# Kernel tuning notes

Measured on AMD Instinct MI355X. Metric: run time of the kernel, lower is better.

Reference implementation:

```python
import jax, jax.numpy as jnp
import numpy as np

C_M = 256
C = 32
N_HEAD = 8
N_SEQ = 256
N_RES = 384


def setup_inputs() -> dict:
    key = jax.random.key(0)
    ks = jax.random.split(key, 10)
    s = 1.0 / np.sqrt(C_M)
    so = 1.0 / np.sqrt(N_HEAD * C)
    return {
        "m": jax.random.normal(ks[0], (N_SEQ, N_RES, C_M), dtype=jnp.float32),
        "ln_gamma": jnp.ones((C_M,), jnp.float32),
        "ln_beta": jnp.zeros((C_M,), jnp.float32),
        "Wq": jax.random.normal(ks[1], (C_M, N_HEAD * C), jnp.float32) * s,
        "Wk": jax.random.normal(ks[2], (C_M, N_HEAD * C), jnp.float32) * s,
        "Wv": jax.random.normal(ks[3], (C_M, N_HEAD * C), jnp.float32) * s,
        "Wg": jax.random.normal(ks[4], (C_M, N_HEAD * C), jnp.float32) * s,
        "bg": jnp.zeros((N_HEAD * C,), jnp.float32),
        "Wo": jax.random.normal(ks[5], (N_HEAD * C, C_M), jnp.float32) * so,
        "bo": jnp.zeros((C_M,), jnp.float32),
    }


def reference(m, ln_gamma, ln_beta, Wq, Wk, Wv, Wg, bg, Wo, bo):
    # LayerNorm over c_m
    mu = jnp.mean(m, axis=-1, keepdims=True)
    var = jnp.mean(jnp.square(m - mu), axis=-1, keepdims=True)
    x = (m - mu) * jax.lax.rsqrt(var + 1e-5) * ln_gamma + ln_beta

    # attention over N_seq axis (attn_dim=-3): move it next to features
    xt = jnp.swapaxes(x, 0, 1)  # (R, S, c_m)
    R, S = xt.shape[0], xt.shape[1]

    def heads(t):  # (R, S, H*c) -> (R, H, S, c)
        return jnp.swapaxes(t.reshape(R, S, N_HEAD, C), 1, 2)

    q = heads(xt @ Wq)
    k = heads(xt @ Wk)
    v = heads(xt @ Wv)

    logits = jnp.einsum("rhqc,rhkc->rhqk", q, k) / jnp.sqrt(jnp.asarray(C, x.dtype))
    attn = jax.nn.softmax(logits, axis=-1)
    o = jnp.einsum("rhqk,rhkc->rhqc", attn, v)  # (R, H, S, c)
    o = jnp.swapaxes(o, 1, 2).reshape(R, S, N_HEAD * C)

    g = jax.nn.sigmoid(xt @ Wg + bg)  # (R, S, H*c)
    out = (g * o) @ Wo + bo  # (R, S, c_m)
    return jnp.swapaxes(out, 0, 1)  # back to (S, R, c_m)
```

## Files before the change

### kernel.cpp

```cpp
#include <hip/hip_runtime.h>
#include <hip/hip_bf16.h>

#define NSEQ 256
#define NRES 384
#define CM   256
#define NH   8
#define HC   32

typedef __bf16 bf16x8_t __attribute__((ext_vector_type(8)));
typedef __bf16 bf16x4_t __attribute__((ext_vector_type(4)));
typedef float  f32x4_t  __attribute__((ext_vector_type(4)));

static __device__ __forceinline__ f32x4_t mfma16(bf16x8_t a, bf16x8_t b, f32x4_t c) {
    return __builtin_amdgcn_mfma_f32_16x16x32_bf16(a, b, c, 0, 0, 0);
}

static __device__ __forceinline__ bf16x4_t to_bf4(f32x4_t v) {
    bf16x4_t o;
    o[0] = (__bf16)v[0]; o[1] = (__bf16)v[1];
    o[2] = (__bf16)v[2]; o[3] = (__bf16)v[3];
    return o;
}

__global__ __launch_bounds__(256) void wprep_kernel(
        const float* __restrict__ wq, const float* __restrict__ wk,
        const float* __restrict__ wv, const float* __restrict__ wg,
        const float* __restrict__ wo, __bf16* __restrict__ wt) {
    const float* src;
    switch (blockIdx.y) {
        case 0: src = wq; break; case 1: src = wk; break;
        case 2: src = wv; break; case 3: src = wg; break;
        default: src = wo; break;
    }
    __bf16* dst = wt + (size_t)blockIdx.y * (CM * CM);
    int n  = blockIdx.x * 16 + (threadIdx.x >> 4);
    int k0 = (threadIdx.x & 15) * 16;
    #pragma unroll
    for (int kk = 0; kk < 16; ++kk) {
        int k = k0 + kk;
        dst[n * CM + k] = (__bf16)src[k * CM + n];
    }
}

__global__ __launch_bounds__(256) void ln_kernel(
        const float* __restrict__ m, const float* __restrict__ gamma,
        const float* __restrict__ beta, __bf16* __restrict__ x) {
    int w = threadIdx.x >> 6, lane = threadIdx.x & 63;
    int row = blockIdx.x * 4 + w;
    const float4 mv = *reinterpret_cast<const float4*>(m + (size_t)row * CM + lane * 4);
    float s1 = mv.x + mv.y + mv.z + mv.w;
    float s2 = mv.x * mv.x + mv.y * mv.y + mv.z * mv.z + mv.w * mv.w;
    #pragma unroll
    for (int d = 1; d < 64; d <<= 1) {
        s1 += __shfl_xor(s1, d);
        s2 += __shfl_xor(s2, d);
    }
    float mu  = s1 * (1.0f / CM);
    float var = s2 * (1.0f / CM) - mu * mu;
    float rs  = rsqrtf(var + 1e-5f);
    const float4 gv = *reinterpret_cast<const float4*>(gamma + lane * 4);
    const float4 bv = *reinterpret_cast<const float4*>(beta + lane * 4);
    int s = row / NRES;
    int r = row - s * NRES;
    int drow = r * NSEQ + s;
    bf16x4_t o;
    o[0] = (__bf16)((mv.x - mu) * rs * gv.x + bv.x);
    o[1] = (__bf16)((mv.y - mu) * rs * gv.y + bv.y);
    o[2] = (__bf16)((mv.z - mu) * rs * gv.z + bv.z);
    o[3] = (__bf16)((mv.w - mu) * rs * gv.w + bv.w);
    *reinterpret_cast<bf16x4_t*>(x + (size_t)drow * CM + lane * 4) = o;
}

__global__ __launch_bounds__(256, 2) void attn_kernel(
        const __bf16* __restrict__ x, const __bf16* __restrict__ wt,
        const float* __restrict__ bg, __bf16* __restrict__ go) {
    const int KRW = 40;
    const int VRW = 264;

    __shared__ __align__(16) char smem[57856];
    __bf16* k_s  = reinterpret_cast<__bf16*>(smem);
    __bf16* q_s  = reinterpret_cast<__bf16*>(smem + 20480);
    __bf16* v_sT = reinterpret_cast<__bf16*>(smem + 40960);

    int tid = threadIdx.x;
    int w = tid >> 6, lane = tid & 63;
    int l15 = lane & 15, g4 = lane >> 4;

    int bid = blockIdx.x;
    int nid = (bid & 7) * 384 + (bid >> 3);
    int r = nid >> 3, h = nid & 7;

    const __bf16* xr = x + (size_t)r * NSEQ * CM;

    const f32x4_t zf = {0.0f, 0.0f, 0.0f, 0.0f};
    f32x4_t acc[4][4][2];
    #pragma unroll
    for (int wi = 0; wi < 4; ++wi)
        #pragma unroll
        for (int mt = 0; mt < 4; ++mt)
            #pragma unroll
            for (int ct = 0; ct < 2; ++ct) acc[wi][mt][ct] = zf;

    #pragma unroll
    for (int kb = 0; kb < 8; ++kb) {
        bf16x8_t a[4];
        #pragma unroll
        for (int mt = 0; mt < 4; ++mt)
            a[mt] = *reinterpret_cast<const bf16x8_t*>(
                xr + (w * 64 + mt * 16 + l15) * CM + kb * 32 + g4 * 8);
        #pragma unroll
        for (int wi = 0; wi < 4; ++wi) {
            const __bf16* wslice = wt + (size_t)wi * (CM * CM) + (h * HC) * CM;
            bf16x8_t b[2];
            #pragma unroll
            for (int ct = 0; ct < 2; ++ct)
                b[ct] = *reinterpret_cast<const bf16x8_t*>(
                    wslice + (ct * 16 + l15) * CM + kb * 32 + g4 * 8);
            #pragma unroll
            for (int mt = 0; mt < 4; ++mt)
                #pragma unroll
                for (int ct = 0; ct < 2; ++ct)
                    acc[wi][mt][ct] = mfma16(a[mt], b[ct], acc[wi][mt][ct]);
        }
    }

    #pragma unroll
    for (int mt = 0; mt < 4; ++mt)
        #pragma unroll
        for (int ct = 0; ct < 2; ++ct) {
            #pragma unroll
            for (int i = 0; i < 4; ++i) {
                q_s[(w * 64 + mt * 16 + g4 * 4 + i) * KRW + ct * 16 + l15] =
                    (__bf16)acc[0][mt][ct][i];
                k_s[(w * 64 + mt * 16 + g4 * 4 + i) * KRW + ct * 16 + l15] =
                    (__bf16)acc[1][mt][ct][i];
            }
            *reinterpret_cast<bf16x4_t*>(
                v_sT + (ct * 16 + l15) * VRW + w * 64 + mt * 16 + g4 * 4) =
                to_bf4(acc[2][mt][ct]);
        }
    __syncthreads();

    bf16x8_t kf[16];
    #pragma unroll
    for (int kt = 0; kt < 16; ++kt)
        kf[kt] = *reinterpret_cast<const bf16x8_t*>(k_s + (kt * 16 + l15) * KRW + g4 * 8);
    bf16x8_t qf[4];
    #pragma unroll
    for (int qt = 0; qt < 4; ++qt)
        qf[qt] = *reinterpret_cast<const bf16x8_t*>(q_s + (w * 64 + qt * 16 + l15) * KRW + g4 * 8);
    __syncthreads();

    __bf16* p_s = reinterpret_cast<__bf16*>(smem + w * 8448);

    float bgv[2];
    bgv[0] = bg[h * HC + l15];
    bgv[1] = bg[h * HC + 16 + l15];
    const float scale = 0.17677669529663687f;

    #pragma unroll
    for (int qt = 0; qt < 4; ++qt) {
        f32x4_t sacc[16];
        #pragma unroll
        for (int kt = 0; kt < 16; ++kt) sacc[kt] = zf;
        #pragma unroll
        for (int kt = 0; kt < 16; ++kt) sacc[kt] = mfma16(kf[kt], qf[qt], sacc[kt]);

        float mx = -1e30f;
        #pragma unroll
        for (int kt = 0; kt < 16; ++kt)
            #pragma unroll
            for (int i = 0; i < 4; ++i) mx = fmaxf(mx, sacc[kt][i]);
        mx = fmaxf(mx, __shfl_xor(mx, 16));
        mx = fmaxf(mx, __shfl_xor(mx, 32));
        float sum = 0.0f;
        #pragma unroll
        for (int kt = 0; kt < 16; ++kt)
            #pragma unroll
            for (int i = 0; i < 4; ++i) {
                float e = __expf((sacc[kt][i] - mx) * scale);
                sacc[kt][i] = e;
                sum += e;
            }
        sum += __shfl_xor(sum, 16);
        sum += __shfl_xor(sum, 32);
        float inv = 1.0f / sum;

        #pragma unroll
        for (int kt = 0; kt < 16; ++kt) {
            bf16x4_t pv;
            #pragma unroll
            for (int i = 0; i < 4; ++i) pv[i] = (__bf16)(sacc[kt][i] * inv);
            *reinterpret_cast<bf16x4_t*>(p_s + l15 * VRW + kt * 16 + g4 * 4) = pv;
        }

        f32x4_t oacc[2];
        oacc[0] = zf; oacc[1] = zf;
        #pragma unroll
        for (int kb = 0; kb < 8; ++kb) {
            bf16x8_t pa = *reinterpret_cast<const bf16x8_t*>(p_s + l15 * VRW + kb * 32 + g4 * 8);
            #pragma unroll
            for (int ct = 0; ct < 2; ++ct) {
                bf16x8_t vb = *reinterpret_cast<const bf16x8_t*>(
                    v_sT + (ct * 16 + l15) * VRW + kb * 32 + g4 * 8);
                oacc[ct] = mfma16(pa, vb, oacc[ct]);
            }
        }

        #pragma unroll
        for (int ct = 0; ct < 2; ++ct)
            #pragma unroll
            for (int i = 0; i < 4; ++i) {
                float t  = acc[3][qt][ct][i] + bgv[ct];
                float gs = 1.0f / (1.0f + __expf(-t));
                int row  = r * NSEQ + w * 64 + qt * 16 + g4 * 4 + i;
                go[(size_t)row * CM + h * HC + ct * 16 + l15] = (__bf16)(gs * oacc[ct][i]);
            }
    }
}

__global__ __launch_bounds__(256, 2) void outgemm_kernel(
        const __bf16* __restrict__ go, const __bf16* __restrict__ wto,
        const float* __restrict__ bo, float* __restrict__ out) {
    int tid = threadIdx.x, w = tid >> 6, lane = tid & 63;
    int l15 = lane & 15, g4 = lane >> 4;
    int j0 = blockIdx.x * 64 + w * 16;
    const f32x4_t zf = {0.0f, 0.0f, 0.0f, 0.0f};
    f32x4_t acc[16];
    #pragma unroll
    for (int nt = 0; nt < 16; ++nt) acc[nt] = zf;
    #pragma unroll
    for (int kb = 0; kb < 8; ++kb) {
        bf16x8_t a = *reinterpret_cast<const bf16x8_t*>(
            go + (size_t)(j0 + l15) * CM + kb * 32 + g4 * 8);
        #pragma unroll
        for (int nt = 0; nt < 16; ++nt) {
            bf16x8_t b = *reinterpret_cast<const bf16x8_t*>(
                wto + (nt * 16 + l15) * CM + kb * 32 + g4 * 8);
            acc[nt] = mfma16(a, b, acc[nt]);
        }
    }
    #pragma unroll
    for (int nt = 0; nt < 16; ++nt) {
        float bias = bo[nt * 16 + l15];
        #pragma unroll
        for (int i = 0; i < 4; ++i) {
            int j = j0 + g4 * 4 + i;
            int s = j & (NSEQ - 1);
            int rr = j >> 8;
            out[((size_t)(s * NRES + rr)) * CM + nt * 16 + l15] = acc[nt][i] + bias;
        }
    }
}

extern "C" void kernel_launch(void* const* d_in, const int* in_sizes, int n_in,
                              void* d_out, int out_size, void* d_ws, size_t ws_size,
                              hipStream_t stream) {
    const float* m     = (const float*)d_in[0];
    const float* gamma = (const float*)d_in[1];
    const float* beta  = (const float*)d_in[2];
    const float* wq    = (const float*)d_in[3];
    const float* wk    = (const float*)d_in[4];
    const float* wv    = (const float*)d_in[5];
    const float* wg    = (const float*)d_in[6];
    const float* bg    = (const float*)d_in[7];
    const float* wo    = (const float*)d_in[8];
    const float* bo    = (const float*)d_in[9];

    char* ws = (char*)d_ws;
    const size_t X_OFF  = 1u << 20;
    const size_t GO_OFF = X_OFF + (size_t)NRES * NSEQ * CM * 2;
    const size_t NEED   = GO_OFF + (size_t)NRES * NSEQ * CM * 2;
    if (ws_size < NEED) return;

    __bf16* wt = (__bf16*)ws;
    __bf16* x  = (__bf16*)(ws + X_OFF);
    __bf16* go = (__bf16*)(ws + GO_OFF);

    wprep_kernel<<<dim3(16, 5), 256, 0, stream>>>(wq, wk, wv, wg, wo, wt);
    ln_kernel<<<(NSEQ * NRES) / 4, 256, 0, stream>>>(m, gamma, beta, x);
    attn_kernel<<<NRES * NH, 256, 0, stream>>>(x, wt, bg, go);
    outgemm_kernel<<<(NRES * NSEQ) / 64, 256, 0, stream>>>(go, wt + 4 * (CM * CM), bo, (float*)d_out);
}
```

Measured before the change: 309.0 us.

## Tile weight transpose, head-major gated output layout, exp2 softmax, MFMA priority

The weight-prep kernel now transposes through a shared-memory tile, so global reads and writes are coalesced instead of strided. The attention kernel writes the gated output in a head-major (r, h, s, c) layout so each head's stores are contiguous, and the output GEMM reads A fragments from that layout. Softmax and sigmoid use exp2 with the scale folded into an FMA. s_setprio is raised around the MFMA loops. These are several unrelated micro-optimizations bundled together; the weight prep is small, so most of any benefit would come from the store-layout change.

```diff
diff --git a/kernel.cpp b/kernel.cpp
--- a/kernel.cpp
+++ b/kernel.cpp
@@ -26,19 +26,27 @@
         const float* __restrict__ wq, const float* __restrict__ wk,
         const float* __restrict__ wv, const float* __restrict__ wg,
         const float* __restrict__ wo, __bf16* __restrict__ wt) {
+    __shared__ float tile[64][65];
     const float* src;
-    switch (blockIdx.y) {
+    switch (blockIdx.z) {
         case 0: src = wq; break; case 1: src = wk; break;
         case 2: src = wv; break; case 3: src = wg; break;
         default: src = wo; break;
     }
-    __bf16* dst = wt + (size_t)blockIdx.y * (CM * CM);
-    int n  = blockIdx.x * 16 + (threadIdx.x >> 4);
-    int k0 = (threadIdx.x & 15) * 16;
-    #pragma unroll
-    for (int kk = 0; kk < 16; ++kk) {
-        int k = k0 + kk;
-        dst[n * CM + k] = (__bf16)src[k * CM + n];
+    __bf16* dst = wt + (size_t)blockIdx.z * (CM * CM);
+    int k0 = blockIdx.x * 64;
+    int n0 = blockIdx.y * 64;
+    int lane = threadIdx.x & 63, wv2 = threadIdx.x >> 6;
+    #pragma unroll
+    for (int i = 0; i < 16; ++i) {
+        int kk = wv2 * 16 + i;
+        tile[kk][lane] = src[(size_t)(k0 + kk) * CM + n0 + lane];
+    }
+    __syncthreads();
+    #pragma unroll
+    for (int i = 0; i < 16; ++i) {
+        int nn = wv2 * 16 + i;
+        dst[(size_t)(n0 + nn) * CM + k0 + lane] = (__bf16)tile[lane][nn];
     }
 }
 
@@ -156,15 +164,20 @@
     float bgv[2];
     bgv[0] = bg[h * HC + l15];
     bgv[1] = bg[h * HC + 16 + l15];
-    const float scale = 0.17677669529663687f;
+    const float cs = 0.17677669529663687f * 1.4426950408889634f;
+    const float l2e = 1.4426950408889634f;
+
+    __bf16* gor = go + (((size_t)r * NH + h) * NSEQ) * HC;
 
     #pragma unroll
     for (int qt = 0; qt < 4; ++qt) {
         f32x4_t sacc[16];
         #pragma unroll
         for (int kt = 0; kt < 16; ++kt) sacc[kt] = zf;
+        __builtin_amdgcn_s_setprio(1);
         #pragma unroll
         for (int kt = 0; kt < 16; ++kt) sacc[kt] = mfma16(kf[kt], qf[qt], sacc[kt]);
+        __builtin_amdgcn_s_setprio(0);
 
         float mx = -1e30f;
         #pragma unroll
@@ -173,12 +186,13 @@
             for (int i = 0; i < 4; ++i) mx = fmaxf(mx, sacc[kt][i]);
         mx = fmaxf(mx, __shfl_xor(mx, 16));
         mx = fmaxf(mx, __shfl_xor(mx, 32));
+        float nmc = -mx * cs;
         float sum = 0.0f;
         #pragma unroll
         for (int kt = 0; kt < 16; ++kt)
             #pragma unroll
             for (int i = 0; i < 4; ++i) {
-                float e = __expf((sacc[kt][i] - mx) * scale);
+                float e = exp2f(__builtin_fmaf(sacc[kt][i], cs, nmc));
                 sacc[kt][i] = e;
                 sum += e;
             }
@@ -196,6 +210,7 @@
 
         f32x4_t oacc[2];
         oacc[0] = zf; oacc[1] = zf;
+        __builtin_amdgcn_s_setprio(1);
         #pragma unroll
         for (int kb = 0; kb < 8; ++kb) {
             bf16x8_t pa = *reinterpret_cast<const bf16x8_t*>(p_s + l15 * VRW + kb * 32 + g4 * 8);
@@ -206,15 +221,16 @@
                 oacc[ct] = mfma16(pa, vb, oacc[ct]);
             }
         }
+        __builtin_amdgcn_s_setprio(0);
 
         #pragma unroll
         for (int ct = 0; ct < 2; ++ct)
             #pragma unroll
             for (int i = 0; i < 4; ++i) {
                 float t  = acc[3][qt][ct][i] + bgv[ct];
-                float gs = 1.0f / (1.0f + __expf(-t));
-                int row  = r * NSEQ + w * 64 + qt * 16 + g4 * 4 + i;
-                go[(size_t)row * CM + h * HC + ct * 16 + l15] = (__bf16)(gs * oacc[ct][i]);
+                float gs = 1.0f / (1.0f + exp2f(-t * l2e));
+                int srow = w * 64 + qt * 16 + g4 * 4 + i;
+                gor[(size_t)srow * HC + ct * 16 + l15] = (__bf16)(gs * oacc[ct][i]);
             }
     }
 }
@@ -225,6 +241,9 @@
     int tid = threadIdx.x, w = tid >> 6, lane = tid & 63;
     int l15 = lane & 15, g4 = lane >> 4;
     int j0 = blockIdx.x * 64 + w * 16;
+    int rb = j0 >> 8;
+    int s0 = j0 & (NSEQ - 1);
+    const __bf16* gor = go + ((size_t)rb * NH) * NSEQ * HC;
     const f32x4_t zf = {0.0f, 0.0f, 0.0f, 0.0f};
     f32x4_t acc[16];
     #pragma unroll
@@ -232,7 +251,7 @@
     #pragma unroll
     for (int kb = 0; kb < 8; ++kb) {
         bf16x8_t a = *reinterpret_cast<const bf16x8_t*>(
-            go + (size_t)(j0 + l15) * CM + kb * 32 + g4 * 8);
+            gor + ((size_t)kb * NSEQ + s0 + l15) * HC + g4 * 8);
         #pragma unroll
         for (int nt = 0; nt < 16; ++nt) {
             bf16x8_t b = *reinterpret_cast<const bf16x8_t*>(
@@ -245,10 +264,8 @@
         float bias = bo[nt * 16 + l15];
         #pragma unroll
         for (int i = 0; i < 4; ++i) {
-            int j = j0 + g4 * 4 + i;
-            int s = j & (NSEQ - 1);
-            int rr = j >> 8;
-            out[((size_t)(s * NRES + rr)) * CM + nt * 16 + l15] = acc[nt][i] + bias;
+            int s = s0 + g4 * 4 + i;
+            out[((size_t)(s * NRES + rb)) * CM + nt * 16 + l15] = acc[nt][i] + bias;
         }
     }
 }
@@ -277,7 +294,7 @@
     __bf16* x  = (__bf16*)(ws + X_OFF);
     __bf16* go = (__bf16*)(ws + GO_OFF);
 
-    wprep_kernel<<<dim3(16, 5), 256, 0, stream>>>(wq, wk, wv, wg, wo, wt);
+    wprep_kernel<<<dim3(4, 4, 5), 256, 0, stream>>>(wq, wk, wv, wg, wo, wt);
     ln_kernel<<<(NSEQ * NRES) / 4, 256, 0, stream>>>(m, gamma, beta, x);
     attn_kernel<<<NRES * NH, 256, 0, stream>>>(x, wt, bg, go);
     outgemm_kernel<<<(NRES * NSEQ) / 64, 256, 0, stream>>>(go, wt + 4 * (CM * CM), bo, (float*)d_out);
```

Result: no change. 307.3 us (-0.6%).
